# Optimization experiments

Hardware: AMD Instinct MI355X
Metric: run time of the kernel (lower is better)

The kernel has to match this reference:

```python
import jax, jax.numpy as jnp
import numpy as np

B, L, D = 1, 1024, 128
EPS = 1e-5


def setup_inputs() -> dict:
    key = jax.random.key(0)
    ks = jax.random.split(key, 10)
    s = 1.0 / np.sqrt(D)
    return {
        "x": jax.random.normal(ks[0], (B, L, D), dtype=jnp.float32),
        "mask": jax.random.randint(ks[1], (B, L, L), 0, 2, dtype=jnp.int32),
        # JCrossOutProduct.l : Linear(D, D)
        "Wl": jax.random.uniform(ks[2], (D, D), jnp.float32, -s, s),
        "bl": jax.random.uniform(ks[3], (D,), jnp.float32, -s, s),
        # JCrossOutProduct.lo : Linear(D, D)
        "Wlo": jax.random.uniform(ks[4], (D, D), jnp.float32, -s, s),
        "blo": jax.random.uniform(ks[5], (D,), jnp.float32, -s, s),
        # JResCOPAttn.l : Linear(D, D)
        "Wl2": jax.random.uniform(ks[6], (D, D), jnp.float32, -s, s),
        "bl2": jax.random.uniform(ks[7], (D,), jnp.float32, -s, s),
        # LayerNorm(D)
        "gamma": jnp.ones((D,), jnp.float32),
        "beta": jnp.zeros((D,), jnp.float32),
    }


def reference(x, mask, Wl, bl, Wlo, blo, Wl2, bl2, gamma, beta):
    # a = self.cop.l(x) : [B, L, D]
    a = x @ Wl.T + bl
    # outer product kept per-channel: [B, L, L, D]
    outer = jnp.einsum('blc,bmc->blmc', a, a)
    # self.cop.lo over last dim: [B, L, L, D]
    tm = outer @ Wlo.T + blo
    # masked_fill(mask.unsqueeze(-1) == 0, 0.0)
    tm = tm * (mask[..., None] != 0).astype(tm.dtype)
    # tx = self.l(x)
    tx = x @ Wl2.T + bl2
    # per-channel attention-like contraction: out[b,c,d] = sum_a tm[b,c,a,d] * tx[b,a,d]
    y = x + jnp.einsum('bcad,bad->bcd', tm, tx)
    # shadow (eval): Dropout=identity, activator 'none'=identity, LayerNorm(D)
    mu = jnp.mean(y, axis=-1, keepdims=True)
    var = jnp.mean(jnp.square(y - mu), axis=-1, keepdims=True)
    return (y - mu) * jax.lax.rsqrt(var + EPS) * gamma + beta
```

## Files before the change

### kernel.cpp

```cpp
#include <hip/hip_runtime.h>
#include <hip/hip_fp16.h>


typedef _Float16 f16x8 __attribute__((ext_vector_type(8)));
typedef float    f32x4 __attribute__((ext_vector_type(4)));

#define LL   1024
#define DD   128
#define EPSV 1e-5f

__global__ __launch_bounds__(256) void prep_kernel(
    const float* __restrict__ x,  const float* __restrict__ Wl,
    const float* __restrict__ bl, const float* __restrict__ Wlo,
    const float* __restrict__ Wl2,const float* __restrict__ bl2,
    _Float16* __restrict__ a_h, float* __restrict__ tx_out,
    _Float16* __restrict__ wh)
{
    __shared__ float xs[16*128];
    __shared__ float wsh[64*132];
    const int t  = threadIdx.x;
    const int bx = blockIdx.x;
    const int by = blockIdx.y;
    const int l0 = by*16;

    #pragma unroll
    for (int i = 0; i < 8; ++i) { int f = i*256 + t; xs[f] = x[l0*DD + f]; }
    const float* Wsrc = ((bx < 2) ? Wl : Wl2) + (bx & 1)*64*DD;
    #pragma unroll
    for (int i = 0; i < 32; ++i) {
        int f = i*256 + t; int r = f >> 7, k = f & 127;
        wsh[r*132 + k] = Wsrc[f];
    }
    __syncthreads();

    const int col  = t & 63;
    const int lsub = t >> 6;
    const float4* W4 = (const float4*)wsh;
    const float4* X4 = (const float4*)xs;
    float acc0 = 0.f, acc1 = 0.f, acc2 = 0.f, acc3 = 0.f;
    #pragma unroll
    for (int k4 = 0; k4 < 32; ++k4) {
        float4 wv = W4[col*33 + k4];
        float4 x0 = X4[(lsub*4+0)*32 + k4];
        float4 x1 = X4[(lsub*4+1)*32 + k4];
        float4 x2 = X4[(lsub*4+2)*32 + k4];
        float4 x3 = X4[(lsub*4+3)*32 + k4];
        acc0 += wv.x*x0.x + wv.y*x0.y + wv.z*x0.z + wv.w*x0.w;
        acc1 += wv.x*x1.x + wv.y*x1.y + wv.z*x1.z + wv.w*x1.w;
        acc2 += wv.x*x2.x + wv.y*x2.y + wv.z*x2.z + wv.w*x2.w;
        acc3 += wv.x*x3.x + wv.y*x3.y + wv.z*x3.z + wv.w*x3.w;
    }
    const int colg = (bx & 1)*64 + col;
    const float bv = ((bx < 2) ? bl : bl2)[colg];
    if (bx < 2) {
        a_h[(l0+lsub*4+0)*DD + colg] = (_Float16)(acc0 + bv);
        a_h[(l0+lsub*4+1)*DD + colg] = (_Float16)(acc1 + bv);
        a_h[(l0+lsub*4+2)*DD + colg] = (_Float16)(acc2 + bv);
        a_h[(l0+lsub*4+3)*DD + colg] = (_Float16)(acc3 + bv);
    } else {
        tx_out[(l0+lsub*4+0)*DD + colg] = acc0 + bv;
        tx_out[(l0+lsub*4+1)*DD + colg] = acc1 + bv;
        tx_out[(l0+lsub*4+2)*DD + colg] = acc2 + bv;
        tx_out[(l0+lsub*4+3)*DD + colg] = acc3 + bv;
    }

    const int gid = (by*4 + bx)*256 + t;
    if (gid < DD*DD) wh[gid] = (_Float16)Wlo[gid];
}

__global__ __launch_bounds__(256, 2) void heavy_kernel(
    const _Float16* __restrict__ a_h, const float* __restrict__ tx,
    const _Float16* __restrict__ wh,  const int* __restrict__ mask,
    const float* __restrict__ blo,    float* __restrict__ part)
{
    __shared__ __align__(16) _Float16 ash[64*DD];
    const int t     = threadIdx.x;
    const int lane  = t & 63, w = t >> 6;
    const int chunk = blockIdx.x;
    const int ltile = blockIdx.y;
    const int l0 = ltile*32, m0 = chunk*64;

    {
        const float4* s4 = (const float4*)(a_h + m0*DD);
        float4* d4 = (float4*)ash;
        #pragma unroll
        for (int i = 0; i < 4; ++i) d4[i*256 + t] = s4[i*256 + t];
    }
    __syncthreads();

    const int grp = lane >> 4, ln = lane & 15;
    const int wl = w >> 1, wd = w & 1;
    const int lbase = l0 + wl*16;
    const int dbase = wd*64;

    f16x8 bh[4][4];
    #pragma unroll
    for (int nf = 0; nf < 4; ++nf)
        #pragma unroll
        for (int k = 0; k < 4; ++k)
            bh[nf][k] = *(const f16x8*)(wh + (dbase + nf*16 + ln)*DD + k*32 + grp*8);

    f16x8 al[4];
    #pragma unroll
    for (int k = 0; k < 4; ++k)
        al[k] = *(const f16x8*)(a_h + (lbase + ln)*DD + k*32 + grp*8);

    float blov[4];
    #pragma unroll
    for (int nf = 0; nf < 4; ++nf) blov[nf] = blo[dbase + nf*16 + ln];

    f32x4 y[4] = {{0,0,0,0},{0,0,0,0},{0,0,0,0},{0,0,0,0}};
    const int mrow0 = lbase + grp*4;

    for (int ml = 0; ml < 64; ++ml) {
        const int mg = m0 + ml;
        float txd[4];
        #pragma unroll
        for (int nf = 0; nf < 4; ++nf) txd[nf] = tx[mg*DD + dbase + nf*16 + ln];
        float wm[4];
        #pragma unroll
        for (int r = 0; r < 4; ++r)
            wm[r] = (mask[(mrow0 + r)*LL + mg] != 0) ? 1.f : 0.f;

        f16x8 ah[4];
        #pragma unroll
        for (int k = 0; k < 4; ++k) {
            f16x8 q = *(const f16x8*)(ash + ml*DD + k*32 + grp*8);
            ah[k] = al[k] * q;
        }

        f32x4 c[4] = {{0,0,0,0},{0,0,0,0},{0,0,0,0},{0,0,0,0}};
        #pragma unroll
        for (int k = 0; k < 4; ++k) {
            c[0] = __builtin_amdgcn_mfma_f32_16x16x32_f16(ah[k], bh[0][k], c[0], 0,0,0);
            c[1] = __builtin_amdgcn_mfma_f32_16x16x32_f16(ah[k], bh[1][k], c[1], 0,0,0);
            c[2] = __builtin_amdgcn_mfma_f32_16x16x32_f16(ah[k], bh[2][k], c[2], 0,0,0);
            c[3] = __builtin_amdgcn_mfma_f32_16x16x32_f16(ah[k], bh[3][k], c[3], 0,0,0);
        }
        #pragma unroll
        for (int nf = 0; nf < 4; ++nf)
            #pragma unroll
            for (int r = 0; r < 4; ++r)
                y[nf][r] += (wm[r]*txd[nf]) * (c[nf][r] + blov[nf]);
    }

    float* dst = part + (size_t)chunk*(LL*DD);
    #pragma unroll
    for (int nf = 0; nf < 4; ++nf)
        #pragma unroll
        for (int r = 0; r < 4; ++r)
            dst[(mrow0 + r)*DD + dbase + nf*16 + ln] = y[nf][r];
}

__global__ __launch_bounds__(128) void finish_kernel(
    const float* __restrict__ x, const float* __restrict__ part,
    const float* __restrict__ gamma, const float* __restrict__ beta,
    float* __restrict__ out)
{
    const int l = blockIdx.x, t = threadIdx.x;
    float v = x[l*DD + t];
    #pragma unroll
    for (int ch = 0; ch < 16; ++ch)
        v += part[((size_t)ch*LL + l)*DD + t];

    float s = v, s2 = v*v;
    #pragma unroll
    for (int o = 32; o > 0; o >>= 1) {
        s  += __shfl_xor(s, o);
        s2 += __shfl_xor(s2, o);
    }
    __shared__ float red[4];
    if ((t & 63) == 0) { red[(t>>6)*2+0] = s; red[(t>>6)*2+1] = s2; }
    __syncthreads();
    const float S  = red[0] + red[2];
    const float S2 = red[1] + red[3];
    const float mu  = S * (1.0f/128.0f);
    const float var = S2 * (1.0f/128.0f) - mu*mu;
    const float inv = rsqrtf(var + EPSV);
    out[l*DD + t] = (v - mu)*inv*gamma[t] + beta[t];
}

extern "C" void kernel_launch(void* const* d_in, const int* in_sizes, int n_in,
                              void* d_out, int out_size, void* d_ws, size_t ws_size,
                              hipStream_t stream)
{
    (void)in_sizes; (void)n_in; (void)out_size; (void)ws_size;
    const float* x     = (const float*)d_in[0];
    const int*   mask  = (const int*)  d_in[1];
    const float* Wl    = (const float*)d_in[2];
    const float* bl    = (const float*)d_in[3];
    const float* Wlo   = (const float*)d_in[4];
    const float* blo   = (const float*)d_in[5];
    const float* Wl2   = (const float*)d_in[6];
    const float* bl2   = (const float*)d_in[7];
    const float* gamma = (const float*)d_in[8];
    const float* beta  = (const float*)d_in[9];
    float* out = (float*)d_out;

    char* ws = (char*)d_ws;
    _Float16* a_h  = (_Float16*)(ws);
    float*    tx_b = (float*)   (ws + (256u<<10));
    _Float16* wh   = (_Float16*)(ws + (768u<<10));
    float*    part = (float*)   (ws + (1024u<<10));

    prep_kernel  <<<dim3(4,64),  256, 0, stream>>>(x, Wl, bl, Wlo, Wl2, bl2,
                                                   a_h, tx_b, wh);
    heavy_kernel <<<dim3(16,32), 256, 0, stream>>>(a_h, tx_b, wh, mask, blo, part);
    finish_kernel<<<1024, 128, 0, stream>>>(x, part, gamma, beta, out);
}
```

Baseline: 122.8 us.

## Stage tx and mask tiles in LDS and factor bias out of inner loop

The heavy kernel now preloads its 64-row tx tile and the 32x64 mask tile into shared memory once per block, so the per-iteration global gathers in the main loop become LDS reads. The bias term is factored algebraically: a running sum of mask*tx weights is kept, and bias times that sum is added once at the end, which removes an add per element per iteration. The prep kernel changes the W tile row pad from 132 to 129 floats and uses scalar LDS loads, presumably to reduce bank conflicts. The loop is also unrolled by two. The cost is more LDS per block (about 56 KB), which may limit occupancy under the 2-blocks-per-SM launch bound, plus extra registers for the S accumulators.

Result: faster. 117.5 us (-4.3%).

```diff
diff --git a/kernel.cpp b/kernel.cpp
--- a/kernel.cpp
+++ b/kernel.cpp
@@ -17,7 +17,7 @@
     _Float16* __restrict__ wh)
 {
     __shared__ float xs[16*128];
-    __shared__ float wsh[64*132];
+    __shared__ float wsh[64*129];
     const int t  = threadIdx.x;
     const int bx = blockIdx.x;
     const int by = blockIdx.y;
@@ -29,18 +29,18 @@
     #pragma unroll
     for (int i = 0; i < 32; ++i) {
         int f = i*256 + t; int r = f >> 7, k = f & 127;
-        wsh[r*132 + k] = Wsrc[f];
+        wsh[r*129 + k] = Wsrc[f];
     }
     __syncthreads();
 
     const int col  = t & 63;
     const int lsub = t >> 6;
-    const float4* W4 = (const float4*)wsh;
     const float4* X4 = (const float4*)xs;
     float acc0 = 0.f, acc1 = 0.f, acc2 = 0.f, acc3 = 0.f;
     #pragma unroll
     for (int k4 = 0; k4 < 32; ++k4) {
-        float4 wv = W4[col*33 + k4];
+        const float* wp = wsh + col*129 + k4*4;
+        float4 wv = {wp[0], wp[1], wp[2], wp[3]};
         float4 x0 = X4[(lsub*4+0)*32 + k4];
         float4 x1 = X4[(lsub*4+1)*32 + k4];
         float4 x2 = X4[(lsub*4+2)*32 + k4];
@@ -74,6 +74,8 @@
     const float* __restrict__ blo,    float* __restrict__ part)
 {
     __shared__ __align__(16) _Float16 ash[64*DD];
+    __shared__ __align__(16) float    txsh[64*DD];
+    __shared__ float                  wmsh[32*64];
     const int t     = threadIdx.x;
     const int lane  = t & 63, w = t >> 6;
     const int chunk = blockIdx.x;
@@ -86,6 +88,20 @@
         #pragma unroll
         for (int i = 0; i < 4; ++i) d4[i*256 + t] = s4[i*256 + t];
     }
+    {
+        const float4* s4 = (const float4*)(tx + m0*DD);
+        float4* d4 = (float4*)txsh;
+        #pragma unroll
+        for (int i = 0; i < 8; ++i) d4[i*256 + t] = s4[i*256 + t];
+    }
+    {
+        #pragma unroll
+        for (int i = 0; i < 8; ++i) {
+            int idx = i*256 + t;
+            int row = idx >> 6, colm = idx & 63;
+            wmsh[idx] = (mask[(l0 + row)*LL + m0 + colm] != 0) ? 1.f : 0.f;
+        }
+    }
     __syncthreads();
 
     const int grp = lane >> 4, ln = lane & 15;
@@ -110,24 +126,23 @@
     for (int nf = 0; nf < 4; ++nf) blov[nf] = blo[dbase + nf*16 + ln];
 
     f32x4 y[4] = {{0,0,0,0},{0,0,0,0},{0,0,0,0},{0,0,0,0}};
+    f32x4 S[4] = {{0,0,0,0},{0,0,0,0},{0,0,0,0},{0,0,0,0}};
     const int mrow0 = lbase + grp*4;
-
+    const int wmbase = (wl*16 + grp*4)*64;
+
+    #pragma unroll 2
     for (int ml = 0; ml < 64; ++ml) {
-        const int mg = m0 + ml;
         float txd[4];
         #pragma unroll
-        for (int nf = 0; nf < 4; ++nf) txd[nf] = tx[mg*DD + dbase + nf*16 + ln];
+        for (int nf = 0; nf < 4; ++nf) txd[nf] = txsh[ml*DD + dbase + nf*16 + ln];
         float wm[4];
         #pragma unroll
-        for (int r = 0; r < 4; ++r)
-            wm[r] = (mask[(mrow0 + r)*LL + mg] != 0) ? 1.f : 0.f;
+        for (int r = 0; r < 4; ++r) wm[r] = wmsh[wmbase + r*64 + ml];
 
         f16x8 ah[4];
         #pragma unroll
-        for (int k = 0; k < 4; ++k) {
-            f16x8 q = *(const f16x8*)(ash + ml*DD + k*32 + grp*8);
-            ah[k] = al[k] * q;
-        }
+        for (int k = 0; k < 4; ++k)
+            ah[k] = al[k] * *(const f16x8*)(ash + ml*DD + k*32 + grp*8);
 
         f32x4 c[4] = {{0,0,0,0},{0,0,0,0},{0,0,0,0},{0,0,0,0}};
         #pragma unroll
@@ -140,8 +155,11 @@
         #pragma unroll
         for (int nf = 0; nf < 4; ++nf)
             #pragma unroll
-            for (int r = 0; r < 4; ++r)
-                y[nf][r] += (wm[r]*txd[nf]) * (c[nf][r] + blov[nf]);
+            for (int r = 0; r < 4; ++r) {
+                float s = wm[r]*txd[nf];
+                y[nf][r] = fmaf(s, c[nf][r], y[nf][r]);
+                S[nf][r] += s;
+            }
     }
 
     float* dst = part + (size_t)chunk*(LL*DD);
@@ -149,7 +167,8 @@
     for (int nf = 0; nf < 4; ++nf)
         #pragma unroll
         for (int r = 0; r < 4; ++r)
-            dst[(mrow0 + r)*DD + dbase + nf*16 + ln] = y[nf][r];
+            dst[(mrow0 + r)*DD + dbase + nf*16 + ln] =
+                fmaf(blov[nf], S[nf][r], y[nf][r]);
 }
 
 __global__ __launch_bounds__(128) void finish_kernel(
```
